# Kernel tuning notes

Hardware: AMD Instinct MI355X
Metric: run time of the kernel (lower is better)

The kernel has to match this reference:

```python
import jax, jax.numpy as jnp
import numpy as np

INDEX_SHIFT = jnp.array([[0, 0], [-1, 0], [1, 0], [0, 1], [-1, 1], [1, 1], [0, -1], [-1, -1], [1, -1]], dtype=jnp.int32)
GRID = jnp.array([513, 513], dtype=jnp.int32)  # pseudo_image_dims + 1


def setup_inputs() -> dict:
    key = jax.random.key(0)
    k1, k2, k3, k4 = jax.random.split(key, 4)
    li_bev_coors = jax.random.randint(k1, (8192, 2), 0, 512, dtype=jnp.int32)
    ra_bev_coors = jax.random.randint(k2, (2048, 2), 0, 512, dtype=jnp.int32)
    ra_pts = jax.random.normal(k3, (2048, 5), dtype=jnp.float32)
    ra_voxel_coords = jax.random.randint(k4, (2048, 3), 0, 512, dtype=jnp.int32)
    return {"li_bev_coors": li_bev_coors, "ra_bev_coors": ra_bev_coors,
            "ra_pts": ra_pts, "ra_voxel_coords": ra_voxel_coords}


def _neighbour_coors(bev_grids):
    # [N,2] -> [N,9,2]: shift by 9-neighborhood, wrap by (grid_size+1)
    return (bev_grids[:, None, :] + INDEX_SHIFT[None, :, :]) % GRID


def _nearest_dy(neighbour_coor, dy_coor, dy_mask):
    # neighbour_coor: [N,9,2] int; dy_coor: [M,2] float; dy_mask: [M] bool
    n = neighbour_coor.shape[0]
    a = neighbour_coor.reshape(-1, 2).astype(jnp.float32)        # [N*9, 2]
    a2 = jnp.sum(a * a, axis=-1)                                  # [N*9]
    b2 = jnp.sum(dy_coor * dy_coor, axis=-1)                      # [M]
    # squared euclidean distances (exact: integer coordinates)
    d2 = a2[:, None] + b2[None, :] - 2.0 * (a @ dy_coor.T)        # [N*9, M]
    d2 = jnp.where(dy_mask[None, :], d2, jnp.inf)                 # mask non-dynamic voxels
    dmin = jnp.sqrt(jnp.maximum(jnp.min(d2, axis=-1), 0.0))       # min commutes with sqrt
    return (dmin * 0.01).reshape(n, 9)


def reference(li_bev_coors, ra_bev_coors, ra_pts, ra_voxel_coords):
    # dynamic-point selection: |velocity| > 0.1 (column 4)
    dy_mask = jnp.abs(ra_pts[:, 4]) > 0.1                         # [M]
    dy_coor = ra_voxel_coords[:, 1:].astype(jnp.float32)          # [M,2]
    # (uniquifying dy_coor does not change the min-distance; skip for jit shapes)
    li_nb = _neighbour_coors(li_bev_coors)                        # [N_li,9,2]
    ra_nb = _neighbour_coors(ra_bev_coors)                        # [N_ra,9,2]
    use = jnp.sum(dy_mask) > 1
    li_dis = jnp.where(use, _nearest_dy(li_nb, dy_coor, dy_mask), 0.0)
    ra_dis = jnp.where(use, _nearest_dy(ra_nb, dy_coor, dy_mask), 0.0)
    return (li_dis, ra_dis)
```

## Files before the change

### kernel.cpp

```cpp
#include <hip/hip_runtime.h>

#define BLOCK 256
#define SPLITS 16
#define QPT 8
#define PREPT 1024



__global__ __launch_bounds__(PREPT) void prep_kernel(
    const float* __restrict__ pts, const int* __restrict__ vox,
    int m, int mPad,
    int* __restrict__ gate, float* __restrict__ wx, float* __restrict__ wy,
    int* __restrict__ out_bits, int total)
{
    __shared__ int s_cnt;
    if (threadIdx.x == 0) s_cnt = 0;
    __syncthreads();

    int nv = 0;
    for (int i = threadIdx.x; i < mPad; i += PREPT) {
        float x = 3.0e4f, y = 3.0e4f;
        if (i < m && fabsf(pts[i * 5 + 4]) > 0.1f) {
            x = (float)vox[i * 3 + 1];
            y = (float)vox[i * 3 + 2];
            nv++;
        }
        wx[i] = x;
        wy[i] = y;
    }
    if (nv) atomicAdd(&s_cnt, nv);

    const int4 iv = make_int4(0x7F7F7F7F, 0x7F7F7F7F, 0x7F7F7F7F, 0x7F7F7F7F);
    int4* o4 = (int4*)out_bits;
    const int n4 = total >> 2;
    for (int i = threadIdx.x; i < n4; i += PREPT) o4[i] = iv;

    __syncthreads();
    if (threadIdx.x == 0) *gate = (s_cnt > 1) ? 1 : 0;
}

__global__ __launch_bounds__(BLOCK) void main_kernel(
    const int* __restrict__ li_coors, int n_li,
    const int* __restrict__ ra_coors, int n_ra,
    const float* __restrict__ wx, const float* __restrict__ wy,
    const int* __restrict__ gate, int cs,
    int* __restrict__ out_bits, int total)
{
    const int split = blockIdx.y;
    const int li_total = n_li * 9;
    const int qbase = blockIdx.x * (BLOCK * QPT) + threadIdx.x;

    float n2x[QPT], n2y[QPT], q2[QPT], mn[QPT];
#pragma unroll
    for (int k = 0; k < QPT; ++k) {
        int q = qbase + k * BLOCK;
        float qx = 0.0f, qy = 0.0f;
        if (q < total) {
            const int shift_x[9] = {0,-1,1,0,-1,1,0,-1,1};
            const int shift_y[9] = {0, 0,0,1, 1,1,-1,-1,-1};
            int n, s;
            const int* src;
            if (q < li_total) { n = q / 9; s = q - n * 9; src = li_coors; }
            else { int r = q - li_total; n = r / 9; s = r - n * 9; src = ra_coors; }
            int cx = src[n * 2 + 0] + shift_x[s];
            int cy = src[n * 2 + 1] + shift_y[s];
            if (cx < 0) cx += 513;
            if (cy < 0) cy += 513;
            qx = (float)cx; qy = (float)cy;
        }
        n2x[k] = -2.0f * qx;
        n2y[k] = -2.0f * qy;
        q2[k]  = fmaf(qx, qx, qy * qy);
        mn[k]  = 3.4e38f;
    }

    const float4* __restrict__ X4 = (const float4*)(wx + split * cs);
    const float4* __restrict__ Y4 = (const float4*)(wy + split * cs);
    const int iters = cs >> 2;
    for (int i = 0; i < iters; ++i) {
        float4 X = X4[i];
        float4 Y = Y4[i];
        float c0 = fmaf(X.x, X.x, Y.x * Y.x);
        float c1 = fmaf(X.y, X.y, Y.y * Y.y);
        float c2 = fmaf(X.z, X.z, Y.z * Y.z);
        float c3 = fmaf(X.w, X.w, Y.w * Y.w);
#pragma unroll
        for (int k = 0; k < QPT; ++k) {
            float t0 = fmaf(X.x, n2x[k], fmaf(Y.x, n2y[k], c0));
            float t1 = fmaf(X.y, n2x[k], fmaf(Y.y, n2y[k], c1));
            float t2 = fmaf(X.z, n2x[k], fmaf(Y.z, n2y[k], c2));
            float t3 = fmaf(X.w, n2x[k], fmaf(Y.w, n2y[k], c3));
            mn[k] = fminf(fminf(t0, t1), mn[k]);
            mn[k] = fminf(fminf(t2, t3), mn[k]);
        }
    }

    const int g = *gate;
#pragma unroll
    for (int k = 0; k < QPT; ++k) {
        int q = qbase + k * BLOCK;
        if (q < total) {
            float d2 = q2[k] + mn[k];
            float val = g ? sqrtf(d2) * 0.01f : 0.0f;
            atomicMin(out_bits + q, __float_as_int(val));
        }
    }
}

extern "C" void kernel_launch(void* const* d_in, const int* in_sizes, int n_in,
                              void* d_out, int out_size, void* d_ws, size_t ws_size,
                              hipStream_t stream) {
    const int*   li  = (const int*)d_in[0];
    const int*   ra  = (const int*)d_in[1];
    const float* pts = (const float*)d_in[2];
    const int*   vox = (const int*)d_in[3];

    const int n_li = in_sizes[0] / 2;
    const int n_ra = in_sizes[1] / 2;
    const int m    = in_sizes[2] / 5;

    const int total = (n_li + n_ra) * 9;
    const int qblocks = (total + BLOCK * QPT - 1) / (BLOCK * QPT);

    const int unit = SPLITS * 4;
    const int mPad = ((m + unit - 1) / unit) * unit;
    const int cs   = mPad / SPLITS;

    int*   gate = (int*)d_ws;
    float* wx   = (float*)((char*)d_ws + 256);
    float* wy   = (float*)((char*)d_ws + 256 + (size_t)mPad * sizeof(float));
    int*   outb = (int*)d_out;

    prep_kernel<<<1, PREPT, 0, stream>>>(pts, vox, m, mPad, gate, wx, wy,
                                         outb, total);
    main_kernel<<<dim3(qblocks, SPLITS), BLOCK, 0, stream>>>(
        li, n_li, ra, n_ra, wx, wy, gate, cs, outb, total);
}
```

Before: 86.00 us.

## Build dynamic-voxel chunks in shared memory and parallelize prep across blocks

Each main-kernel block now builds its own chunk of masked voxel coordinates directly into shared memory, which removes the global wx/wy staging buffers written by the prep kernel. The prep kernel becomes a multi-block launch that only fills the output with the min sentinel and computes the dynamic-count gate in block 0. This shortens the serial single-block prep, at the cost of every query block redundantly reading pts/vox for its split. Chunk size is capped by MAXC, which fixes the maximum m per split, and the inner loop gains an unroll pragma.

```diff
diff --git a/kernel.cpp b/kernel.cpp
--- a/kernel.cpp
+++ b/kernel.cpp
@@ -3,50 +3,58 @@
 #define BLOCK 256
 #define SPLITS 16
 #define QPT 8
-#define PREPT 1024
+#define PREPB 90
+#define MAXC 136
 
 
-
-__global__ __launch_bounds__(PREPT) void prep_kernel(
-    const float* __restrict__ pts, const int* __restrict__ vox,
-    int m, int mPad,
-    int* __restrict__ gate, float* __restrict__ wx, float* __restrict__ wy,
-    int* __restrict__ out_bits, int total)
+__global__ __launch_bounds__(BLOCK) void prep_kernel(
+    const float* __restrict__ pts, int m,
+    int* __restrict__ gate, int* __restrict__ out_bits, int total)
 {
     __shared__ int s_cnt;
-    if (threadIdx.x == 0) s_cnt = 0;
-    __syncthreads();
-
-    int nv = 0;
-    for (int i = threadIdx.x; i < mPad; i += PREPT) {
-        float x = 3.0e4f, y = 3.0e4f;
-        if (i < m && fabsf(pts[i * 5 + 4]) > 0.1f) {
-            x = (float)vox[i * 3 + 1];
-            y = (float)vox[i * 3 + 2];
-            nv++;
-        }
-        wx[i] = x;
-        wy[i] = y;
-    }
-    if (nv) atomicAdd(&s_cnt, nv);
-
+    const int tid = blockIdx.x * BLOCK + threadIdx.x;
+    const int n4 = total >> 2;
     const int4 iv = make_int4(0x7F7F7F7F, 0x7F7F7F7F, 0x7F7F7F7F, 0x7F7F7F7F);
     int4* o4 = (int4*)out_bits;
-    const int n4 = total >> 2;
-    for (int i = threadIdx.x; i < n4; i += PREPT) o4[i] = iv;
+    for (int i = tid; i < n4; i += PREPB * BLOCK) o4[i] = iv;
 
-    __syncthreads();
-    if (threadIdx.x == 0) *gate = (s_cnt > 1) ? 1 : 0;
+    if (blockIdx.x == 0) {
+        if (threadIdx.x == 0) s_cnt = 0;
+        __syncthreads();
+        int nv = 0;
+        for (int i = threadIdx.x; i < m; i += BLOCK)
+            nv += (fabsf(pts[i * 5 + 4]) > 0.1f) ? 1 : 0;
+        if (nv) atomicAdd(&s_cnt, nv);
+        __syncthreads();
+        if (threadIdx.x == 0) *gate = (s_cnt > 1) ? 1 : 0;
+    }
 }
 
 __global__ __launch_bounds__(BLOCK) void main_kernel(
     const int* __restrict__ li_coors, int n_li,
     const int* __restrict__ ra_coors, int n_ra,
-    const float* __restrict__ wx, const float* __restrict__ wy,
-    const int* __restrict__ gate, int cs,
+    const float* __restrict__ pts,
+    const int* __restrict__ vox,
+    int m, int cs, int csPad,
+    const int* __restrict__ gate,
     int* __restrict__ out_bits, int total)
 {
-    const int split = blockIdx.y;
+    __shared__ __align__(16) float sx[MAXC];
+    __shared__ __align__(16) float sy[MAXC];
+
+    const int base = blockIdx.y * cs;
+    for (int i = threadIdx.x; i < csPad; i += BLOCK) {
+        int gi = base + i;
+        float x = 3.0e4f, y = 3.0e4f;
+        if (i < cs && gi < m && fabsf(pts[gi * 5 + 4]) > 0.1f) {
+            x = (float)vox[gi * 3 + 1];
+            y = (float)vox[gi * 3 + 2];
+        }
+        sx[i] = x;
+        sy[i] = y;
+    }
+    __syncthreads();
+
     const int li_total = n_li * 9;
     const int qbase = blockIdx.x * (BLOCK * QPT) + threadIdx.x;
 
@@ -74,9 +82,10 @@
         mn[k]  = 3.4e38f;
     }
 
-    const float4* __restrict__ X4 = (const float4*)(wx + split * cs);
-    const float4* __restrict__ Y4 = (const float4*)(wy + split * cs);
-    const int iters = cs >> 2;
+    const float4* __restrict__ X4 = (const float4*)sx;
+    const float4* __restrict__ Y4 = (const float4*)sy;
+    const int iters = csPad >> 2;
+#pragma unroll 4
     for (int i = 0; i < iters; ++i) {
         float4 X = X4[i];
         float4 Y = Y4[i];
@@ -100,8 +109,7 @@
     for (int k = 0; k < QPT; ++k) {
         int q = qbase + k * BLOCK;
         if (q < total) {
-            float d2 = q2[k] + mn[k];
-            float val = g ? sqrtf(d2) * 0.01f : 0.0f;
+            float val = g ? sqrtf(q2[k] + mn[k]) * 0.01f : 0.0f;
             atomicMin(out_bits + q, __float_as_int(val));
         }
     }
@@ -122,17 +130,13 @@
     const int total = (n_li + n_ra) * 9;
     const int qblocks = (total + BLOCK * QPT - 1) / (BLOCK * QPT);
 
-    const int unit = SPLITS * 4;
-    const int mPad = ((m + unit - 1) / unit) * unit;
-    const int cs   = mPad / SPLITS;
+    const int cs    = (m + SPLITS - 1) / SPLITS;
+    const int csPad = (cs + 3) & ~3;
 
-    int*   gate = (int*)d_ws;
-    float* wx   = (float*)((char*)d_ws + 256);
-    float* wy   = (float*)((char*)d_ws + 256 + (size_t)mPad * sizeof(float));
-    int*   outb = (int*)d_out;
+    int* gate = (int*)d_ws;
+    int* outb = (int*)d_out;
 
-    prep_kernel<<<1, PREPT, 0, stream>>>(pts, vox, m, mPad, gate, wx, wy,
-                                         outb, total);
+    prep_kernel<<<PREPB, BLOCK, 0, stream>>>(pts, m, gate, outb, total);
     main_kernel<<<dim3(qblocks, SPLITS), BLOCK, 0, stream>>>(
-        li, n_li, ra, n_ra, wx, wy, gate, cs, outb, total);
+        li, n_li, ra, n_ra, pts, vox, m, cs, csPad, gate, outb, total);
 }
```

New measurement: 79.18 us. 7.9% less time.
